# Performance work log

Hardware: AMD Instinct MI355X
Metric: run time of the kernel (lower is better)

Reference implementation:

```python
import jax, jax.numpy as jnp
import numpy as np

N_NODES = 100000
N_EDGES = 1600000
D_IN = 128
D_HID = 256
D_OUT = 128


def _glorot(key, shape):
    fan_in, fan_out = shape[1], shape[0]
    lim = (6.0 / (fan_in + fan_out)) ** 0.5
    return jax.random.uniform(key, shape, jnp.float32, -lim, lim)


def setup_inputs() -> dict:
    key = jax.random.key(0)
    ks = jax.random.split(key, 8)
    x = jax.random.normal(ks[0], (N_NODES, D_IN), jnp.float32)
    edge_index = jax.random.randint(ks[1], (2, N_EDGES), 0, N_NODES, jnp.int32)
    return {
        "x": x,
        "edge_index": edge_index,
        # layer 1: in=D_IN -> D_HID
        "Wl1": _glorot(ks[2], (D_HID, D_IN)), "bl1": jnp.zeros((D_HID,), jnp.float32),
        "Wr1": _glorot(ks[3], (D_HID, D_IN)),
        # layer 2: D_HID -> D_HID
        "Wl2": _glorot(ks[4], (D_HID, D_HID)), "bl2": jnp.zeros((D_HID,), jnp.float32),
        "Wr2": _glorot(ks[5], (D_HID, D_HID)),
        # layer 3: D_HID -> D_OUT
        "Wl3": _glorot(ks[6], (D_OUT, D_HID)), "bl3": jnp.zeros((D_OUT,), jnp.float32),
        "Wr3": _glorot(ks[7], (D_OUT, D_HID)),
    }


def _sage_conv(x, src, dst, inv_deg, Wl, bl, Wr):
    # PyG SAGEConv (aggr='mean'): out = lin_l(mean_j x_j) + lin_r(x_i)
    agg = jax.ops.segment_sum(x[src], dst, num_segments=N_NODES)  # [N, F]
    mean = agg * inv_deg[:, None]
    return mean @ Wl.T + bl + x @ Wr.T


def reference(x, edge_index, Wl1, bl1, Wr1, Wl2, bl2, Wr2, Wl3, bl3, Wr3):
    src, dst = edge_index[0], edge_index[1]
    deg = jax.ops.segment_sum(jnp.ones((src.shape[0],), jnp.float32), dst,
                              num_segments=N_NODES)
    inv_deg = jnp.where(deg > 0, 1.0 / jnp.maximum(deg, 1.0), 0.0)
    h = jax.nn.relu(_sage_conv(x, src, dst, inv_deg, Wl1, bl1, Wr1))
    h = jax.nn.relu(_sage_conv(h, src, dst, inv_deg, Wl2, bl2, Wr2))
    return _sage_conv(h, src, dst, inv_deg, Wl3, bl3, Wr3)
```

## Files before the change

### kernel.cpp

```cpp
#include <hip/hip_runtime.h>

#define NN 100000
#define NE 1600000
#define DIN 128
#define DHID 256
#define DOUT 128
#define CAP 64

typedef unsigned int u32;
typedef unsigned short u16;

typedef __bf16 bf16x8 __attribute__((ext_vector_type(8)));
typedef float  f32x4  __attribute__((ext_vector_type(4)));

__device__ inline u16 f2bf(float f) {
    u32 u = __float_as_uint(f);
    u32 r = u + 0x7FFFu + ((u >> 16) & 1u);
    return (u16)(r >> 16);
}
__device__ inline u32 pack2(float a, float b) {
    return (u32)f2bf(a) | ((u32)f2bf(b) << 16);
}
__device__ inline float bflo(u32 u) { return __uint_as_float(u << 16); }
__device__ inline float bfhi(u32 u) { return __uint_as_float(u & 0xffff0000u); }

__global__ void csr_build(const int* __restrict__ src, const int* __restrict__ dst,
                          int* __restrict__ fill, int* __restrict__ csrC, int nE) {
    int g  = blockIdx.x & 7;
    int bg = blockIdx.x >> 3;
    int nbg = gridDim.x >> 3;
    int lo = g * (NN / 8), hi = lo + (NN / 8);
    for (int e = bg * 256 + threadIdx.x; e < nE; e += nbg * 256) {
        int d = __builtin_nontemporal_load(dst + e);
        if (d >= lo && d < hi) {
            int pos = atomicAdd(&fill[d], 1);
            if (pos < CAP) csrC[(size_t)d * CAP + pos] = __builtin_nontemporal_load(src + e);
        }
    }
}

__global__ void conv_all(const float4* __restrict__ x,
                         const float4* __restrict__ W0, const float4* __restrict__ W1,
                         const float4* __restrict__ W2, const float4* __restrict__ W3,
                         const float4* __restrict__ W4, const float4* __restrict__ W5,
                         uint2* __restrict__ x_out, uint2* __restrict__ w_out) {
    int i = blockIdx.x * 256 + threadIdx.x;
    const int XT = NN * 32;
    if (i < XT) {
        float4 v = x[i];
        uint2 r; r.x = pack2(v.x, v.y); r.y = pack2(v.z, v.w);
        x_out[i] = r;
        return;
    }
    int j = i - XT;
    if (j >= 65536) return;
    const float4* p; int off;
    if (j < 8192)       { p = W0; off = j; }
    else if (j < 16384) { p = W1; off = j - 8192; }
    else if (j < 32768) { p = W2; off = j - 16384; }
    else if (j < 49152) { p = W3; off = j - 32768; }
    else if (j < 57344) { p = W4; off = j - 49152; }
    else                { p = W5; off = j - 57344; }
    float4 v = p[off];
    uint2 r; r.x = pack2(v.x, v.y); r.y = pack2(v.z, v.w);
    w_out[j] = r;
}

#define ACC8(A, U) \
    A[0] += bflo(U.x); A[1] += bfhi(U.x); A[2] += bflo(U.y); A[3] += bfhi(U.y); \
    A[4] += bflo(U.z); A[5] += bfhi(U.z); A[6] += bflo(U.w); A[7] += bfhi(U.w);

__global__ __launch_bounds__(256)
void agg128_u4(const uint4* __restrict__ feat,
               const int* __restrict__ fill,
               const int* __restrict__ csrC, uint4* __restrict__ aggOut) {
    int w = (blockIdx.x * 256 + threadIdx.x) >> 6;
    int lane = threadIdx.x & 63;
    if (w >= NN) return;
    int dgt = fill[w];
    float iv = dgt > 0 ? 1.0f / (float)dgt : 0.0f;
    int dg = dgt > CAP ? CAP : dgt;
    const int* cp = csrC + (size_t)w * CAP;
    int q = lane >> 4, sub = lane & 15;
    float a[8] = {0,0,0,0,0,0,0,0};
    float b[8] = {0,0,0,0,0,0,0,0};
    int j = 0;
    for (; j + 7 < dg; j += 8) {
        int s0 = cp[j + q], s1 = cp[j + 4 + q];
        uint4 u0 = feat[(size_t)s0 * 16 + sub];
        uint4 u1 = feat[(size_t)s1 * 16 + sub];
        ACC8(a, u0); ACC8(b, u1);
    }
    while (j < dg) {
        if (j + q < dg) {
            int s0 = cp[j + q];
            uint4 u0 = feat[(size_t)s0 * 16 + sub];
            ACC8(a, u0);
        }
        j += 4;
    }
#pragma unroll
    for (int i = 0; i < 8; ++i) {
        float v = a[i] + b[i];
        v += __shfl_xor(v, 16, 64);
        v += __shfl_xor(v, 32, 64);
        a[i] = v * iv;
    }
    if (q == 0) {
        uint4 r;
        r.x = pack2(a[0], a[1]); r.y = pack2(a[2], a[3]);
        r.z = pack2(a[4], a[5]); r.w = pack2(a[6], a[7]);
        aggOut[(size_t)w * 16 + sub] = r;
    }
}

__global__ __launch_bounds__(256)
void agg256_u4(const uint4* __restrict__ feat,
               const int* __restrict__ fill,
               const int* __restrict__ csrC, uint4* __restrict__ aggOut) {
    int w = (blockIdx.x * 256 + threadIdx.x) >> 6;
    int lane = threadIdx.x & 63;
    if (w >= NN) return;
    int dgt = fill[w];
    float iv = dgt > 0 ? 1.0f / (float)dgt : 0.0f;
    int dg = dgt > CAP ? CAP : dgt;
    const int* cp = csrC + (size_t)w * CAP;
    int h = lane >> 5, sub = lane & 31;
    float a[8] = {0,0,0,0,0,0,0,0};
    float b[8] = {0,0,0,0,0,0,0,0};
    float c[8] = {0,0,0,0,0,0,0,0};
    float d[8] = {0,0,0,0,0,0,0,0};
    int j = 0;
    for (; j + 7 < dg; j += 8) {
        int s0 = cp[j + h],     s1 = cp[j + 2 + h];
        int s2 = cp[j + 4 + h], s3 = cp[j + 6 + h];
        uint4 u0 = feat[(size_t)s0 * 32 + sub];
        uint4 u1 = feat[(size_t)s1 * 32 + sub];
        uint4 u2 = feat[(size_t)s2 * 32 + sub];
        uint4 u3 = feat[(size_t)s3 * 32 + sub];
        ACC8(a, u0); ACC8(b, u1); ACC8(c, u2); ACC8(d, u3);
    }
    while (j < dg) {
        if (j + h < dg) {
            int s0 = cp[j + h];
            uint4 u0 = feat[(size_t)s0 * 32 + sub];
            ACC8(a, u0);
        }
        j += 2;
    }
#pragma unroll
    for (int i = 0; i < 8; ++i) {
        float v = (a[i] + b[i]) + (c[i] + d[i]);
        v += __shfl_xor(v, 32, 64);
        a[i] = v * iv;
    }
    if (h == 0) {
        uint4 r;
        r.x = pack2(a[0], a[1]); r.y = pack2(a[2], a[3]);
        r.z = pack2(a[4], a[5]); r.w = pack2(a[6], a[7]);
        aggOut[(size_t)w * 32 + sub] = r;
    }
}

template<int SH, int OFF>
__global__ __launch_bounds__(256)
void agg_bf16(const u32* __restrict__ feat,
              const int* __restrict__ fill,
              const int* __restrict__ csrC, u32* __restrict__ aggOut) {
    int w = (blockIdx.x * 256 + threadIdx.x) >> 6;
    int lane = threadIdx.x & 63;
    if (w >= NN) return;
    int dgt = fill[w];
    float iv = dgt > 0 ? 1.0f / (float)dgt : 0.0f;
    int dg = dgt > CAP ? CAP : dgt;
    const int* cp = csrC + (size_t)w * CAP;
    float a0 = 0.f, b0 = 0.f, a1 = 0.f, b1 = 0.f;
    int j = 0;
    for (; j + 1 < dg; j += 2) {
        int s0 = cp[j], s1 = cp[j+1];
        u32 u0 = feat[((size_t)s0 << SH) + OFF + lane];
        u32 u1 = feat[((size_t)s1 << SH) + OFF + lane];
        a0 += bflo(u0); b0 += bfhi(u0);
        a1 += bflo(u1); b1 += bfhi(u1);
    }
    if (j < dg) {
        u32 u0 = feat[((size_t)cp[j] << SH) + OFF + lane];
        a0 += bflo(u0); b0 += bfhi(u0);
    }
    aggOut[(size_t)w * 64 + lane] = pack2((a0 + a1) * iv, (b0 + b1) * iv);
}

#define TM 128
#define TN 128
#define TK 32
#define LDSTR 40

__device__ inline void mfma_pass_bf(const u16* __restrict__ A, int K, int lda,
                                    const u16* __restrict__ Wb, int ldw,
                                    int brow, int bcol, int n,
                                    int tid, int lane, int wr, int wc,
                                    u16* As, u16* Ws, f32x4 (&acc)[4][4])
{
    int rsel = lane & 15;
    int krun = (lane >> 4) << 3;
    int r0 = tid >> 2,         k80 = (tid & 3) << 3;
    int r1 = (tid + 256) >> 2, k81 = k80;
    uint4 av0, av1, wv0, wv1;
    const uint4 zero4 = make_uint4(0u, 0u, 0u, 0u);

    av0 = (brow + r0 < n) ? *(const uint4*)(A + (size_t)(brow + r0) * lda + k80) : zero4;
    av1 = (brow + r1 < n) ? *(const uint4*)(A + (size_t)(brow + r1) * lda + k81) : zero4;
    wv0 = *(const uint4*)(Wb + (size_t)(bcol + r0) * ldw + k80);
    wv1 = *(const uint4*)(Wb + (size_t)(bcol + r1) * ldw + k81);

    for (int kt = 0; kt < K; kt += TK) {
        __syncthreads();
        *(uint4*)&As[r0 * LDSTR + k80] = av0;
        *(uint4*)&As[r1 * LDSTR + k81] = av1;
        *(uint4*)&Ws[r0 * LDSTR + k80] = wv0;
        *(uint4*)&Ws[r1 * LDSTR + k81] = wv1;
        __syncthreads();
        int kn = kt + TK;
        if (kn < K) {
            av0 = (brow + r0 < n) ? *(const uint4*)(A + (size_t)(brow + r0) * lda + kn + k80) : zero4;
            av1 = (brow + r1 < n) ? *(const uint4*)(A + (size_t)(brow + r1) * lda + kn + k81) : zero4;
            wv0 = *(const uint4*)(Wb + (size_t)(bcol + r0) * ldw + kn + k80);
            wv1 = *(const uint4*)(Wb + (size_t)(bcol + r1) * ldw + kn + k81);
        }
        bf16x8 a[4], b[4];
#pragma unroll
        for (int mb = 0; mb < 4; ++mb)
            a[mb] = *(const bf16x8*)&As[(64 * wr + 16 * mb + rsel) * LDSTR + krun];
#pragma unroll
        for (int nb = 0; nb < 4; ++nb)
            b[nb] = *(const bf16x8*)&Ws[(64 * wc + 16 * nb + rsel) * LDSTR + krun];
#pragma unroll
        for (int mb = 0; mb < 4; ++mb)
#pragma unroll
            for (int nb = 0; nb < 4; ++nb)
                acc[mb][nb] = __builtin_amdgcn_mfma_f32_16x16x32_bf16(
                    a[mb], b[nb], acc[mb][nb], 0, 0, 0);
    }
}

template<int CF32, int RELU, int ACCUM>
__global__ __launch_bounds__(256)
void gemm_mfma(const u16* __restrict__ A1, int K1, int lda1,
               const u16* __restrict__ W1, int ldw1,
               const u16* __restrict__ A2, int K2, int lda2,
               const u16* __restrict__ W2, int ldw2,
               const float* __restrict__ bias, const u16* __restrict__ accBuf,
               void* __restrict__ C, int n, int cout)
{
    __shared__ u16 As[TM * LDSTR];
    __shared__ u16 Ws[TN * LDSTR];
    int tid = threadIdx.x;
    int lane = tid & 63, wid = tid >> 6;
    int wr = wid >> 1, wc = wid & 1;
    int brow = blockIdx.x * TM, bcol = blockIdx.y * TN;

    f32x4 acc[4][4];
#pragma unroll
    for (int i = 0; i < 4; ++i)
#pragma unroll
        for (int j = 0; j < 4; ++j) acc[i][j] = (f32x4){0.f, 0.f, 0.f, 0.f};

    mfma_pass_bf(A1, K1, lda1, W1, ldw1, brow, bcol, n, tid, lane, wr, wc, As, Ws, acc);
    if (K2 > 0)
        mfma_pass_bf(A2, K2, lda2, W2, ldw2, brow, bcol, n, tid, lane, wr, wc, As, Ws, acc);

    int rsel = lane & 15;
    int rgrp = (lane >> 4) << 2;
    float bv[4];
#pragma unroll
    for (int nb = 0; nb < 4; ++nb)
        bv[nb] = bias ? bias[bcol + 64 * wc + 16 * nb + rsel] : 0.f;

#pragma unroll
    for (int mb = 0; mb < 4; ++mb) {
        int rowb = brow + 64 * wr + 16 * mb + rgrp;
#pragma unroll
        for (int r = 0; r < 4; ++r) {
            int row = rowb + r;
            if (row >= n) continue;
            size_t rof = (size_t)row * cout;
#pragma unroll
            for (int nb = 0; nb < 4; ++nb) {
                int col = bcol + 64 * wc + 16 * nb + rsel;
                float v = acc[mb][nb][r] + bv[nb];
                if (ACCUM == 2) v += __uint_as_float(((u32)accBuf[rof + col]) << 16);
                if (CF32) {
                    float* p = (float*)C + rof + col;
                    if (ACCUM == 1) v += *p;
                    if (RELU) v = fmaxf(v, 0.f);
                    *p = v;
                } else {
                    u16* p = (u16*)C + rof + col;
                    if (ACCUM == 1) v += __uint_as_float(((u32)(*p)) << 16);
                    if (RELU) v = fmaxf(v, 0.f);
                    *p = f2bf(v);
                }
            }
        }
    }
}

extern "C" void kernel_launch(void* const* d_in, const int* in_sizes, int n_in,
                              void* d_out, int out_size, void* d_ws, size_t ws_size,
                              hipStream_t stream) {
    const float* x   = (const float*)d_in[0];
    const int*   ei  = (const int*)d_in[1];
    const float* Wl1 = (const float*)d_in[2];
    const float* bl1 = (const float*)d_in[3];
    const float* Wr1 = (const float*)d_in[4];
    const float* Wl2 = (const float*)d_in[5];
    const float* bl2 = (const float*)d_in[6];
    const float* Wr2 = (const float*)d_in[7];
    const float* Wl3 = (const float*)d_in[8];
    const float* bl3 = (const float*)d_in[9];
    const float* Wr3 = (const float*)d_in[10];
    float* out = (float*)d_out;

    const int* src = ei;
    const int* dst = ei + NE;

    char* ws = (char*)d_ws;
    int*   fill   = (int*)  (ws + 0);
    int*   csrC   = (int*)  (ws + 800000);
    u16*   Wb     = (u16*)  (ws + 26400000);
    u16*   aggS   = (u16*)  (ws + 26924288);
    u16*   h2     = (u16*)  (ws + 52524288);
    u16*   h1     = (u16*)  (ws + 103724288);
    u16*   agg256 = (u16*)  (ws + 154924288);
    u16*   x_bf   = h2;
    u16*   t3     = h1;

    const bool big = ws_size >= 206124288ull;

    u16* wbL1 = Wb + 0;
    u16* wbR1 = Wb + 32768;
    u16* wbL2 = Wb + 65536;
    u16* wbR2 = Wb + 131072;
    u16* wbL3 = Wb + 196608;
    u16* wbR3 = Wb + 229376;

    dim3 b256(256);
    dim3 gW((NN * 64 + 255) / 256);
    dim3 gConv((NN * 32 + 65536 + 255) / 256);
    dim3 gg2((NN + TM - 1) / TM, DHID / TN);
    dim3 gg1((NN + TM - 1) / TM, DOUT / TN);

    hipLaunchKernelGGL(conv_all, gConv, b256, 0, stream,
                       (const float4*)x,
                       (const float4*)Wl1, (const float4*)Wr1, (const float4*)Wl2,
                       (const float4*)Wr2, (const float4*)Wl3, (const float4*)Wr3,
                       (uint2*)x_bf, (uint2*)Wb);

    hipMemsetAsync(fill, 0, 400000, stream);
    hipLaunchKernelGGL(csr_build, dim3(2048), b256, 0, stream, src, dst, fill, csrC, NE);

    hipLaunchKernelGGL(agg128_u4, gW, b256, 0, stream,
                       (const uint4*)x_bf, fill, csrC, (uint4*)aggS);
    hipLaunchKernelGGL((gemm_mfma<0, 1, 0>), gg2, b256, 0, stream,
                       aggS, DIN, DIN, wbL1, DIN,
                       x_bf, DIN, DIN, wbR1, DIN,
                       bl1, nullptr, h1, NN, DHID);

    if (big) {
        hipLaunchKernelGGL(agg256_u4, gW, b256, 0, stream,
                           (const uint4*)h1, fill, csrC, (uint4*)agg256);
        hipLaunchKernelGGL((gemm_mfma<0, 1, 0>), gg2, b256, 0, stream,
                           agg256, DHID, DHID, wbL2, DHID,
                           h1, DHID, DHID, wbR2, DHID,
                           bl2, nullptr, h2, NN, DHID);
    } else {
        hipLaunchKernelGGL((agg_bf16<7, 0>), gW, b256, 0, stream,
                           (const u32*)h1, fill, csrC, (u32*)aggS);
        hipLaunchKernelGGL((gemm_mfma<0, 0, 0>), gg2, b256, 0, stream,
                           aggS, 128, 128, wbL2, DHID,
                           h1, DHID, DHID, wbR2, DHID,
                           bl2, nullptr, h2, NN, DHID);
        hipLaunchKernelGGL((agg_bf16<7, 64>), gW, b256, 0, stream,
                           (const u32*)h1, fill, csrC, (u32*)aggS);
        hipLaunchKernelGGL((gemm_mfma<0, 1, 1>), gg2, b256, 0, stream,
                           aggS, 128, 128, wbL2 + 128, DHID,
                           nullptr, 0, 0, nullptr, 0,
                           nullptr, nullptr, h2, NN, DHID);
    }

    hipLaunchKernelGGL((gemm_mfma<0, 0, 0>), gg1, b256, 0, stream,
                       h2, DHID, DHID, wbL3, DHID,
                       nullptr, 0, 0, nullptr, 0,
                       nullptr, nullptr, t3, NN, DOUT);
    hipLaunchKernelGGL(agg128_u4, gW, b256, 0, stream,
                       (const uint4*)t3, fill, csrC, (uint4*)aggS);
    hipLaunchKernelGGL((gemm_mfma<1, 0, 2>), gg1, b256, 0, stream,
                       h2, DHID, DHID, wbR3, DHID,
                       nullptr, 0, 0, nullptr, 0,
                       bl3, aggS, out, NN, DOUT);
}
```

Measured before the change: 474.8 us.

## Bind CSR-build node ranges to XCDs via hardware XCC id and work stealing

```diff
diff --git a/kernel.cpp b/kernel.cpp
--- a/kernel.cpp
+++ b/kernel.cpp
@@ -6,6 +6,8 @@
 #define DHID 256
 #define DOUT 128
 #define CAP 64
+#define CHUNK 4096
+#define NCHUNK ((NE + CHUNK - 1) / CHUNK)
 
 typedef unsigned int u32;
 typedef unsigned short u16;
@@ -24,17 +26,41 @@
 __device__ inline float bflo(u32 u) { return __uint_as_float(u << 16); }
 __device__ inline float bfhi(u32 u) { return __uint_as_float(u & 0xffff0000u); }
 
-__global__ void csr_build(const int* __restrict__ src, const int* __restrict__ dst,
-                          int* __restrict__ fill, int* __restrict__ csrC, int nE) {
-    int g  = blockIdx.x & 7;
-    int bg = blockIdx.x >> 3;
-    int nbg = gridDim.x >> 3;
-    int lo = g * (NN / 8), hi = lo + (NN / 8);
-    for (int e = bg * 256 + threadIdx.x; e < nE; e += nbg * 256) {
-        int d = __builtin_nontemporal_load(dst + e);
-        if (d >= lo && d < hi) {
-            int pos = atomicAdd(&fill[d], 1);
-            if (pos < CAP) csrC[(size_t)d * CAP + pos] = __builtin_nontemporal_load(src + e);
+__device__ inline int get_xcd() {
+    int x;
+    asm volatile("s_getreg_b32 %0, hwreg(HW_REG_XCC_ID)" : "=s"(x));
+    return x & 7;
+}
+
+__global__ void csr_build_xcd(const int* __restrict__ src, const int* __restrict__ dst,
+                              int* __restrict__ fill, int* __restrict__ csrC,
+                              int* __restrict__ ctr) {
+    int xcd = get_xcd();
+    __shared__ int sTask;
+    for (;;) {
+        if (threadIdx.x == 0) {
+            int task = -1;
+            for (int pass = 0; pass < 8; ++pass) {
+                int g = (xcd + pass) & 7;
+                int t = atomicAdd(&ctr[g], 1);
+                if (t < NCHUNK) { task = g * NCHUNK + t; break; }
+            }
+            sTask = task;
+        }
+        __syncthreads();
+        int task = sTask;
+        __syncthreads();
+        if (task < 0) return;
+        int g = task / NCHUNK, c = task - g * NCHUNK;
+        int lo = g * (NN / 8), hi = lo + (NN / 8);
+        int e0 = c * CHUNK;
+        int e1 = e0 + CHUNK; if (e1 > NE) e1 = NE;
+        for (int e = e0 + threadIdx.x; e < e1; e += 256) {
+            int d = __builtin_nontemporal_load(dst + e);
+            if (d >= lo && d < hi) {
+                int pos = atomicAdd(&fill[d], 1);
+                if (pos < CAP) csrC[(size_t)d * CAP + pos] = __builtin_nontemporal_load(src + e);
+            }
         }
     }
 }
@@ -326,6 +352,7 @@
 
     char* ws = (char*)d_ws;
     int*   fill   = (int*)  (ws + 0);
+    int*   ctr    = (int*)  (ws + 400000);
     int*   csrC   = (int*)  (ws + 800000);
     u16*   Wb     = (u16*)  (ws + 26400000);
     u16*   aggS   = (u16*)  (ws + 26924288);
@@ -356,8 +383,9 @@
                        (const float4*)Wr2, (const float4*)Wl3, (const float4*)Wr3,
                        (uint2*)x_bf, (uint2*)Wb);
 
-    hipMemsetAsync(fill, 0, 400000, stream);
-    hipLaunchKernelGGL(csr_build, dim3(2048), b256, 0, stream, src, dst, fill, csrC, NE);
+    hipMemsetAsync(fill, 0, 400032, stream);
+    hipLaunchKernelGGL(csr_build_xcd, dim3(2048), b256, 0, stream,
+                       src, dst, fill, csrC, ctr);
 
     hipLaunchKernelGGL(agg128_u4, gW, b256, 0, stream,
                        (const uint4*)x_bf, fill, csrC, (uint4*)aggS);
```

Measured after the change: 668.0 us. 1.41x slower.
